# Optimization experiments

Measured on AMD Instinct MI355X. Metric: run time of the kernel, lower is better.

Reference implementation:

```python
import jax, jax.numpy as jnp
import numpy as np

N_NODE = 100000
HIDDEN = 128
BATCH = 4096
SESS_LEN = 50


def setup_inputs() -> dict:
    key = jax.random.key(0)
    k1, k2, k3, k4, k5 = jax.random.split(key, 5)
    return {
        "item_embedding": jax.random.normal(k1, (N_NODE, HIDDEN), dtype=jnp.float32),
        "items": jax.random.randint(k2, (BATCH, SESS_LEN), 0, N_NODE, dtype=jnp.int64),
        "A": jax.random.uniform(k3, (BATCH, BATCH), dtype=jnp.float32),
        "D": jax.random.uniform(k4, (BATCH, BATCH), dtype=jnp.float32),
        "target_embedding": jax.random.normal(k5, (BATCH, 1, 2 * HIDDEN), dtype=jnp.float32),
    }


def reference(item_embedding, items, A, D, target_embedding):
    # Gather per-session item embeddings: (batch, sess_len, hidden)
    seq_h = item_embedding[items]
    # Sum over session positions -> (batch, hidden)
    relation_emb = jnp.sum(seq_h, axis=1)
    # DA = D @ A, then propagate: (batch, batch) @ (batch, hidden)
    DA = jnp.matmul(D, A)
    relation_emb = jnp.matmul(DA, relation_emb)
    # Row-wise L2 normalization (torch.norm(dim=-1))
    norm = jnp.linalg.norm(relation_emb, axis=-1, keepdims=True)
    return relation_emb / norm
```

## Files before the change

### kernel.cpp

```cpp
#include <hip/hip_runtime.h>
#include <hip/hip_bf16.h>

#define BATCH   4096
#define HIDDEN  128
#define SESS    50
#define KTOT    4096
#define NB      ((size_t)BATCH * HIDDEN)

#define BK      128
#define NTILES  (KTOT / BK)
#define ABYTES  8192
#define BBYTES  32768
#define BUF     (ABYTES + BBYTES)

typedef __bf16 bf16x8 __attribute__((ext_vector_type(8)));
typedef __bf16 bf16x4 __attribute__((ext_vector_type(4)));
typedef float  f32x4  __attribute__((ext_vector_type(4)));

__device__ __forceinline__ f32x4 mfma_bf16(bf16x8 a, bf16x8 b, f32x4 c) {
    return __builtin_amdgcn_mfma_f32_16x16x32_bf16(a, b, c, 0, 0, 0);
}

__device__ __forceinline__ void gload16(const void* g, void* l) {
    __builtin_amdgcn_global_load_lds(
        (const __attribute__((address_space(1))) void*)g,
        (__attribute__((address_space(3))) void*)l, 16, 0, 0);
}


__global__ __launch_bounds__(256)
void gather_sum_kernel(const float* __restrict__ emb,
                       const int* __restrict__ items32,
                       __bf16* __restrict__ ETp) {
    __shared__ int sidx[4][SESS];
    const int t  = threadIdx.x;
    const int b0 = blockIdx.x * 4;
    const bool is64 = (items32[1] | items32[3] | items32[5] | items32[7] |
                       items32[9] | items32[11] | items32[13] | items32[15]) == 0;
    if (t < 4 * SESS) {
        const int w_ = t / SESS, s_ = t % SESS;
        sidx[w_][s_] = is64
            ? (int)((const long long*)items32)[(long)(b0 + w_) * SESS + s_]
            : items32[(b0 + w_) * SESS + s_];
    }
    __syncthreads();
    const int w    = t >> 6;
    const int lane = t & 63;
    const int c    = lane & 31;
    const int h    = lane >> 5;
    f32x4 acc = {0.f, 0.f, 0.f, 0.f};
#pragma unroll
    for (int i = 0; i < 25; ++i) {
        acc += *(const f32x4*)(emb + (long)sidx[w][h + 2 * i] * HIDDEN + c * 4);
    }
#pragma unroll
    for (int j = 0; j < 4; ++j) acc[j] += __shfl_xor(acc[j], 32, 64);
    if (h == 0) {
        const int  b     = b0 + w;
        const long chunk = b >> 3;
        const int  swz   = (int)((chunk & 3) << 4);
        char* basep = (char*)ETp + chunk * 2048 + (b & 7) * 2;
        const int hi4 = (c >> 2) * 256;
#pragma unroll
        for (int j = 0; j < 4; ++j) {
            const int hl = 4 * (c & 3) + j;
            *(__bf16*)(basep + ((hi4 + hl * 16) ^ swz)) = (__bf16)acc[j];
        }
    }
}

template <int PHASE>
__global__ __launch_bounds__(256, 1)
void gemm_mfma_kernel(const float* __restrict__ X,
                      const __bf16* __restrict__ Bpk,
                      __bf16* __restrict__ TTp,
                      float* __restrict__ out) {
    __shared__ __align__(16) char lds[3 * BUF];
    const int tid  = threadIdx.x;
    const int w    = tid >> 6;
    const int lane = tid & 63;
    const int lo   = lane & 15;
    const int quad = lane >> 4;
    const int rowBase = blockIdx.x * 16;

#define STAGE(t_, dst_) do {                                                 \
    _Pragma("unroll")                                                        \
    for (int oi_ = 0; oi_ < 2; ++oi_) {                                      \
        const int o_    = 2 * w + oi_;                                       \
        const int rloc_ = 2 * o_ + (lane >> 5);                              \
        gload16((const char*)X +                                             \
                    ((size_t)(rowBase + rloc_) * KTOT + (size_t)(t_) * BK) * 4 + \
                    (((lane & 31) * 16) ^ ((rloc_ & 7) << 4)),               \
                (dst_) + o_ * 1024);                                         \
    }                                                                        \
    _Pragma("unroll")                                                        \
    for (int bi_ = 0; bi_ < 8; ++bi_) {                                      \
        const int i_ = 8 * w + bi_;                                          \
        gload16((const char*)Bpk + (size_t)(t_) * BBYTES + i_ * 1024 +       \
                    lane * 16,                                               \
                (dst_) + ABYTES + i_ * 1024);                                \
    }                                                                        \
} while (0)

    f32x4 acc0 = {0.f, 0.f, 0.f, 0.f};
    f32x4 acc1 = {0.f, 0.f, 0.f, 0.f};

    const int akey = (lo & 7) << 4;
    const int bswz = quad << 4;
    const int bc0  = (int)(((2 * w) * 256 + lo * 16) ^ bswz);
    const int bc1  = (int)(((2 * w + 1) * 256 + lo * 16) ^ bswz);

#define KTILE(cb_) do {                                                      \
    const char* Ar_ = (cb_) + lo * 512;                                      \
    const char* Bb_ = (cb_) + ABYTES + quad * 2048;                          \
    _Pragma("unroll")                                                        \
    for (int ks_ = 0; ks_ < 4; ++ks_) {                                      \
        const f32x4 a0_ =                                                    \
            *(const f32x4*)(Ar_ + ((ks_ * 128 + quad * 32) ^ akey));         \
        const f32x4 a1_ =                                                    \
            *(const f32x4*)(Ar_ + ((ks_ * 128 + quad * 32 + 16) ^ akey));    \
        const bf16x8 b0_ = *(const bf16x8*)(Bb_ + ks_ * 8192 + bc0);         \
        const bf16x8 b1_ = *(const bf16x8*)(Bb_ + ks_ * 8192 + bc1);         \
        bf16x8 af_;                                                          \
        af_[0] = (__bf16)a0_[0]; af_[1] = (__bf16)a0_[1];                    \
        af_[2] = (__bf16)a0_[2]; af_[3] = (__bf16)a0_[3];                    \
        af_[4] = (__bf16)a1_[0]; af_[5] = (__bf16)a1_[1];                    \
        af_[6] = (__bf16)a1_[2]; af_[7] = (__bf16)a1_[3];                    \
        acc0 = mfma_bf16(af_, b0_, acc0);                                    \
        acc1 = mfma_bf16(af_, b1_, acc1);                                    \
    }                                                                        \
} while (0)

    STAGE(0, lds);
    STAGE(1, lds + BUF);

    char* cb = lds;
    char* sb = lds + 2 * BUF;
    for (int t = 0; t < NTILES; ++t) {
        if (t + 2 < NTILES) STAGE(t + 2, sb);
        if (t < NTILES - 2)
            asm volatile("s_waitcnt vmcnt(20)" ::: "memory");
        else if (t == NTILES - 2)
            asm volatile("s_waitcnt vmcnt(10)" ::: "memory");
        else
            asm volatile("s_waitcnt vmcnt(0)" ::: "memory");
        __builtin_amdgcn_s_barrier();
        __builtin_amdgcn_sched_barrier(0);
        KTILE(cb);
        __builtin_amdgcn_s_barrier();
        __builtin_amdgcn_sched_barrier(0);
        cb += BUF; if (cb == lds + 3 * BUF) cb = lds;
        sb += BUF; if (sb == lds + 3 * BUF) sb = lds;
    }
#undef KTILE
#undef STAGE

    if (PHASE == 1) {
        const long chunk = (rowBase >> 3) + (quad >> 1);
        const int  swz   = (int)((chunk & 3) << 4);
        char* tb = (char*)TTp + chunk * 2048 + (quad & 1) * 8;
        bf16x4 p0, p1;
#pragma unroll
        for (int r = 0; r < 4; ++r) {
            p0[r] = (__bf16)acc0[r];
            p1[r] = (__bf16)acc1[r];
        }
        *(bf16x4*)(tb + (((2 * w) * 256 + lo * 16) ^ swz))     = p0;
        *(bf16x4*)(tb + (((2 * w + 1) * 256 + lo * 16) ^ swz)) = p1;
    } else {
        __syncthreads();
        float (*Cs)[136] = (float (*)[136])lds;
#pragma unroll
        for (int r = 0; r < 4; ++r) {
            Cs[quad * 4 + r][(2 * w) * 16 + lo]     = acc0[r];
            Cs[quad * 4 + r][(2 * w + 1) * 16 + lo] = acc1[r];
        }
        __syncthreads();
        const int row = tid >> 4;
        const int cg  = tid & 15;
        const f32x4 c0 = *(const f32x4*)&Cs[row][cg * 8];
        const f32x4 c1 = *(const f32x4*)&Cs[row][cg * 8 + 4];
        float sq = c0[0] * c0[0] + c0[1] * c0[1] + c0[2] * c0[2] +
                   c0[3] * c0[3] + c1[0] * c1[0] + c1[1] * c1[1] +
                   c1[2] * c1[2] + c1[3] * c1[3];
#pragma unroll
        for (int m = 1; m < 16; m <<= 1) sq += __shfl_xor(sq, m, 64);
        const float s = rsqrtf(sq);
        float* op = out + (size_t)(rowBase + row) * HIDDEN + cg * 8;
        f32x4 o0, o1;
#pragma unroll
        for (int j = 0; j < 4; ++j) { o0[j] = c0[j] * s; o1[j] = c1[j] * s; }
        *(f32x4*)(op)     = o0;
        *(f32x4*)(op + 4) = o1;
    }
}

extern "C" void kernel_launch(void* const* d_in, const int* in_sizes, int n_in,
                              void* d_out, int out_size, void* d_ws, size_t ws_size,
                              hipStream_t stream) {
    const float* emb   = (const float*)d_in[0];
    const int*   items = (const int*)d_in[1];
    const float* A     = (const float*)d_in[2];
    const float* D     = (const float*)d_in[3];
    float* out = (float*)d_out;

    __bf16* ETp = (__bf16*)d_ws;
    __bf16* TTp = ETp + NB;

    gather_sum_kernel<<<BATCH / 4, 256, 0, stream>>>(emb, items, ETp);
    gemm_mfma_kernel<1><<<BATCH / 16, 256, 0, stream>>>(A, ETp, TTp, nullptr);
    gemm_mfma_kernel<2><<<BATCH / 16, 256, 0, stream>>>(D, TTp, nullptr, out);
}
```

Measured before the change: 207.9 us.

## Split-K GEMMs in two with 32-row tiles and separate reduce kernels

Each GEMM block now covers 32 output rows instead of 16, which halves how often the B operand is reloaded per row. Each wave computes a 16x64 subtile with four accumulators. The K dimension is split in two across blockIdx.y, which keeps the grid at 256 blocks and writes fp32 partial sums to workspace. Two new small kernels add the partials: one packs the intermediate to swizzled bf16 and the other applies the row L2 normalization. This costs two extra launches and an extra fp32 round-trip through global memory.

Measured after the change: 209.8 us. No clear change (+0.9%).

```diff
diff --git a/kernel.cpp b/kernel.cpp
--- a/kernel.cpp
+++ b/kernel.cpp
@@ -8,14 +8,15 @@
 #define NB      ((size_t)BATCH * HIDDEN)
 
 #define BK      128
-#define NTILES  (KTOT / BK)
-#define ABYTES  8192
+#define NT      16
+#define ABYTES  16384
 #define BBYTES  32768
 #define BUF     (ABYTES + BBYTES)
 
 typedef __bf16 bf16x8 __attribute__((ext_vector_type(8)));
 typedef __bf16 bf16x4 __attribute__((ext_vector_type(4)));
 typedef float  f32x4  __attribute__((ext_vector_type(4)));
+typedef float  f32x2  __attribute__((ext_vector_type(2)));
 
 __device__ __forceinline__ f32x4 mfma_bf16(bf16x8 a, bf16x8 b, f32x4 c) {
     return __builtin_amdgcn_mfma_f32_16x16x32_bf16(a, b, c, 0, 0, 0);
@@ -69,49 +70,50 @@
     }
 }
 
-template <int PHASE>
 __global__ __launch_bounds__(256, 1)
 void gemm_mfma_kernel(const float* __restrict__ X,
                       const __bf16* __restrict__ Bpk,
-                      __bf16* __restrict__ TTp,
-                      float* __restrict__ out) {
+                      float* __restrict__ Tpart) {
     __shared__ __align__(16) char lds[3 * BUF];
     const int tid  = threadIdx.x;
     const int w    = tid >> 6;
     const int lane = tid & 63;
     const int lo   = lane & 15;
     const int quad = lane >> 4;
-    const int rowBase = blockIdx.x * 16;
+    const int rowBase = blockIdx.x * 32;
+    const int kh      = blockIdx.y;
 
 #define STAGE(t_, dst_) do {                                                 \
     _Pragma("unroll")                                                        \
-    for (int oi_ = 0; oi_ < 2; ++oi_) {                                      \
-        const int o_    = 2 * w + oi_;                                       \
-        const int rloc_ = 2 * o_ + (lane >> 5);                              \
+    for (int ai_ = 0; ai_ < 4; ++ai_) {                                      \
+        const int i_    = 4 * w + ai_;                                       \
+        const int rloc_ = 2 * i_ + (lane >> 5);                              \
         gload16((const char*)X +                                             \
-                    ((size_t)(rowBase + rloc_) * KTOT + (size_t)(t_) * BK) * 4 + \
+                    ((size_t)(rowBase + rloc_) * KTOT + kh * 2048 +          \
+                     (size_t)(t_) * BK) * 4 +                                \
                     (((lane & 31) * 16) ^ ((rloc_ & 7) << 4)),               \
-                (dst_) + o_ * 1024);                                         \
+                (dst_) + i_ * 1024);                                         \
     }                                                                        \
     _Pragma("unroll")                                                        \
     for (int bi_ = 0; bi_ < 8; ++bi_) {                                      \
-        const int i_ = 8 * w + bi_;                                          \
-        gload16((const char*)Bpk + (size_t)(t_) * BBYTES + i_ * 1024 +       \
-                    lane * 16,                                               \
-                (dst_) + ABYTES + i_ * 1024);                                \
+        const int j_ = 8 * w + bi_;                                          \
+        gload16((const char*)Bpk + (size_t)kh * 524288 +                     \
+                    (size_t)(t_) * BBYTES + j_ * 1024 + lane * 16,           \
+                (dst_) + ABYTES + j_ * 1024);                                \
     }                                                                        \
 } while (0)
 
-    f32x4 acc0 = {0.f, 0.f, 0.f, 0.f};
-    f32x4 acc1 = {0.f, 0.f, 0.f, 0.f};
-
-    const int akey = (lo & 7) << 4;
-    const int bswz = quad << 4;
-    const int bc0  = (int)(((2 * w) * 256 + lo * 16) ^ bswz);
-    const int bc1  = (int)(((2 * w + 1) * 256 + lo * 16) ^ bswz);
+    f32x4 acc[4];
+#pragma unroll
+    for (int i = 0; i < 4; ++i) acc[i] = (f32x4){0.f, 0.f, 0.f, 0.f};
+
+    const int rbase = (w & 1) * 16;
+    const int ntb   = (w >> 1) * 4;
+    const int akey  = (lo & 7) << 4;
+    const int bkey  = quad << 4;
 
 #define KTILE(cb_) do {                                                      \
-    const char* Ar_ = (cb_) + lo * 512;                                      \
+    const char* Ar_ = (cb_) + (rbase + lo) * 512;                            \
     const char* Bb_ = (cb_) + ABYTES + quad * 2048;                          \
     _Pragma("unroll")                                                        \
     for (int ks_ = 0; ks_ < 4; ++ks_) {                                      \
@@ -119,15 +121,17 @@
             *(const f32x4*)(Ar_ + ((ks_ * 128 + quad * 32) ^ akey));         \
         const f32x4 a1_ =                                                    \
             *(const f32x4*)(Ar_ + ((ks_ * 128 + quad * 32 + 16) ^ akey));    \
-        const bf16x8 b0_ = *(const bf16x8*)(Bb_ + ks_ * 8192 + bc0);         \
-        const bf16x8 b1_ = *(const bf16x8*)(Bb_ + ks_ * 8192 + bc1);         \
         bf16x8 af_;                                                          \
         af_[0] = (__bf16)a0_[0]; af_[1] = (__bf16)a0_[1];                    \
         af_[2] = (__bf16)a0_[2]; af_[3] = (__bf16)a0_[3];                    \
         af_[4] = (__bf16)a1_[0]; af_[5] = (__bf16)a1_[1];                    \
         af_[6] = (__bf16)a1_[2]; af_[7] = (__bf16)a1_[3];                    \
-        acc0 = mfma_bf16(af_, b0_, acc0);                                    \
-        acc1 = mfma_bf16(af_, b1_, acc1);                                    \
+        _Pragma("unroll")                                                    \
+        for (int j_ = 0; j_ < 4; ++j_) {                                     \
+            const bf16x8 b_ = *(const bf16x8*)(Bb_ + ks_ * 8192 +            \
+                (((ntb + j_) * 256 + lo * 16) ^ bkey));                      \
+            acc[j_] = mfma_bf16(af_, b_, acc[j_]);                           \
+        }                                                                    \
     }                                                                        \
 } while (0)
 
@@ -136,12 +140,12 @@
 
     char* cb = lds;
     char* sb = lds + 2 * BUF;
-    for (int t = 0; t < NTILES; ++t) {
-        if (t + 2 < NTILES) STAGE(t + 2, sb);
-        if (t < NTILES - 2)
-            asm volatile("s_waitcnt vmcnt(20)" ::: "memory");
-        else if (t == NTILES - 2)
-            asm volatile("s_waitcnt vmcnt(10)" ::: "memory");
+    for (int t = 0; t < NT; ++t) {
+        if (t + 2 < NT) STAGE(t + 2, sb);
+        if (t < NT - 2)
+            asm volatile("s_waitcnt vmcnt(24)" ::: "memory");
+        else if (t == NT - 2)
+            asm volatile("s_waitcnt vmcnt(12)" ::: "memory");
         else
             asm volatile("s_waitcnt vmcnt(0)" ::: "memory");
         __builtin_amdgcn_s_barrier();
@@ -155,44 +159,49 @@
 #undef KTILE
 #undef STAGE
 
-    if (PHASE == 1) {
-        const long chunk = (rowBase >> 3) + (quad >> 1);
-        const int  swz   = (int)((chunk & 3) << 4);
-        char* tb = (char*)TTp + chunk * 2048 + (quad & 1) * 8;
-        bf16x4 p0, p1;
-#pragma unroll
-        for (int r = 0; r < 4; ++r) {
-            p0[r] = (__bf16)acc0[r];
-            p1[r] = (__bf16)acc1[r];
-        }
-        *(bf16x4*)(tb + (((2 * w) * 256 + lo * 16) ^ swz))     = p0;
-        *(bf16x4*)(tb + (((2 * w + 1) * 256 + lo * 16) ^ swz)) = p1;
-    } else {
-        __syncthreads();
-        float (*Cs)[136] = (float (*)[136])lds;
-#pragma unroll
-        for (int r = 0; r < 4; ++r) {
-            Cs[quad * 4 + r][(2 * w) * 16 + lo]     = acc0[r];
-            Cs[quad * 4 + r][(2 * w + 1) * 16 + lo] = acc1[r];
-        }
-        __syncthreads();
-        const int row = tid >> 4;
-        const int cg  = tid & 15;
-        const f32x4 c0 = *(const f32x4*)&Cs[row][cg * 8];
-        const f32x4 c1 = *(const f32x4*)&Cs[row][cg * 8 + 4];
-        float sq = c0[0] * c0[0] + c0[1] * c0[1] + c0[2] * c0[2] +
-                   c0[3] * c0[3] + c1[0] * c1[0] + c1[1] * c1[1] +
-                   c1[2] * c1[2] + c1[3] * c1[3];
-#pragma unroll
-        for (int m = 1; m < 16; m <<= 1) sq += __shfl_xor(sq, m, 64);
-        const float s = rsqrtf(sq);
-        float* op = out + (size_t)(rowBase + row) * HIDDEN + cg * 8;
-        f32x4 o0, o1;
-#pragma unroll
-        for (int j = 0; j < 4; ++j) { o0[j] = c0[j] * s; o1[j] = c1[j] * s; }
-        *(f32x4*)(op)     = o0;
-        *(f32x4*)(op + 4) = o1;
-    }
+    float* op = Tpart + (size_t)kh * NB +
+                (size_t)(rowBase + rbase) * HIDDEN;
+#pragma unroll
+    for (int r = 0; r < 4; ++r) {
+#pragma unroll
+        for (int j = 0; j < 4; ++j)
+            op[(quad * 4 + r) * HIDDEN + (ntb + j) * 16 + lo] = acc[j][r];
+    }
+}
+
+__global__ __launch_bounds__(256)
+void reduce2_kernel(const float* __restrict__ Tp, __bf16* __restrict__ TTp) {
+    const size_t i = ((size_t)blockIdx.x * 256 + threadIdx.x) * 4;
+    f32x4 a = *(const f32x4*)(Tp + i);
+    a += *(const f32x4*)(Tp + NB + i);
+    const int  b     = (int)(i >> 7);
+    const int  h0    = (int)(i & 127);
+    const long chunk = b >> 3;
+    const int  swz   = (int)((chunk & 3) << 4);
+    char* basep = (char*)TTp + chunk * 2048 + (b & 7) * 2;
+#pragma unroll
+    for (int j = 0; j < 4; ++j) {
+        const int h = h0 + j;
+        *(__bf16*)(basep + (((h >> 4) * 256 + (h & 15) * 16) ^ swz)) =
+            (__bf16)a[j];
+    }
+}
+
+__global__ __launch_bounds__(256)
+void reduce_norm_kernel(const float* __restrict__ Tp, float* __restrict__ out) {
+    const int t    = threadIdx.x;
+    const int w    = t >> 6;
+    const int lane = t & 63;
+    const int row  = blockIdx.x * 4 + w;
+    const size_t base = (size_t)row * HIDDEN + lane * 2;
+    f32x2 v = *(const f32x2*)(Tp + base);
+    v += *(const f32x2*)(Tp + NB + base);
+    float sq = v[0] * v[0] + v[1] * v[1];
+#pragma unroll
+    for (int m = 1; m < 64; m <<= 1) sq += __shfl_xor(sq, m, 64);
+    const float s = rsqrtf(sq);
+    f32x2 o = {v[0] * s, v[1] * s};
+    *(f32x2*)(out + base) = o;
 }
 
 extern "C" void kernel_launch(void* const* d_in, const int* in_sizes, int n_in,
@@ -206,8 +215,11 @@
 
     __bf16* ETp = (__bf16*)d_ws;
     __bf16* TTp = ETp + NB;
+    float*  Tp  = (float*)(TTp + NB);
 
     gather_sum_kernel<<<BATCH / 4, 256, 0, stream>>>(emb, items, ETp);
-    gemm_mfma_kernel<1><<<BATCH / 16, 256, 0, stream>>>(A, ETp, TTp, nullptr);
-    gemm_mfma_kernel<2><<<BATCH / 16, 256, 0, stream>>>(D, TTp, nullptr, out);
-}
+    gemm_mfma_kernel<<<dim3(BATCH / 32, 2), 256, 0, stream>>>(A, ETp, Tp);
+    reduce2_kernel<<<512, 256, 0, stream>>>(Tp, TTp);
+    gemm_mfma_kernel<<<dim3(BATCH / 32, 2), 256, 0, stream>>>(D, TTp, Tp);
+    reduce_norm_kernel<<<BATCH / 4, 256, 0, stream>>>(Tp, out);
+}
```

## Fuse gather and both GEMMs into one cooperative kernel with grid syncs

Applied to the files above, without the earlier changes.

Merges the gather-sum kernel and the two chained GEMMs into a single cooperative launch of 512 blocks, separated by grid-wide syncs. Each GEMM block now covers a 16x64 output tile instead of 16x128, which doubles the block count and allows two blocks per CU. The row normalization moves to a final phase that reads an fp32 intermediate buffer. This removes two kernel launch gaps and improves occupancy, at the cost of grid-sync overhead, an extra global round trip for the result, and re-reading the A/D rows twice (once per N-half).

Measured after the change: 592.8 us. +185.1%, slower.

```diff
diff --git a/kernel.cpp b/kernel.cpp
--- a/kernel.cpp
+++ b/kernel.cpp
@@ -1,5 +1,8 @@
 #include <hip/hip_runtime.h>
 #include <hip/hip_bf16.h>
+#include <hip/hip_cooperative_groups.h>
+
+namespace cg = cooperative_groups;
 
 #define BATCH   4096
 #define HIDDEN  128
@@ -8,14 +11,15 @@
 #define NB      ((size_t)BATCH * HIDDEN)
 
 #define BK      128
-#define NTILES  (KTOT / BK)
-#define ABYTES  8192
-#define BBYTES  32768
-#define BUF     (ABYTES + BBYTES)
+#define NT      (KTOT / BK)
+#define ABY     8192
+#define BBY     16384
+#define BUF     (ABY + BBY)
 
 typedef __bf16 bf16x8 __attribute__((ext_vector_type(8)));
 typedef __bf16 bf16x4 __attribute__((ext_vector_type(4)));
 typedef float  f32x4  __attribute__((ext_vector_type(4)));
+typedef float  f32x2  __attribute__((ext_vector_type(2)));
 
 __device__ __forceinline__ f32x4 mfma_bf16(bf16x8 a, bf16x8 b, f32x4 c) {
     return __builtin_amdgcn_mfma_f32_16x16x32_bf16(a, b, c, 0, 0, 0);
@@ -28,170 +32,174 @@
 }
 
 
-__global__ __launch_bounds__(256)
-void gather_sum_kernel(const float* __restrict__ emb,
-                       const int* __restrict__ items32,
-                       __bf16* __restrict__ ETp) {
-    __shared__ int sidx[4][SESS];
-    const int t  = threadIdx.x;
-    const int b0 = blockIdx.x * 4;
-    const bool is64 = (items32[1] | items32[3] | items32[5] | items32[7] |
-                       items32[9] | items32[11] | items32[13] | items32[15]) == 0;
-    if (t < 4 * SESS) {
-        const int w_ = t / SESS, s_ = t % SESS;
-        sidx[w_][s_] = is64
-            ? (int)((const long long*)items32)[(long)(b0 + w_) * SESS + s_]
-            : items32[(b0 + w_) * SESS + s_];
-    }
-    __syncthreads();
-    const int w    = t >> 6;
-    const int lane = t & 63;
-    const int c    = lane & 31;
-    const int h    = lane >> 5;
-    f32x4 acc = {0.f, 0.f, 0.f, 0.f};
-#pragma unroll
-    for (int i = 0; i < 25; ++i) {
-        acc += *(const f32x4*)(emb + (long)sidx[w][h + 2 * i] * HIDDEN + c * 4);
-    }
-#pragma unroll
-    for (int j = 0; j < 4; ++j) acc[j] += __shfl_xor(acc[j], 32, 64);
-    if (h == 0) {
-        const int  b     = b0 + w;
-        const long chunk = b >> 3;
-        const int  swz   = (int)((chunk & 3) << 4);
-        char* basep = (char*)ETp + chunk * 2048 + (b & 7) * 2;
-        const int hi4 = (c >> 2) * 256;
-#pragma unroll
-        for (int j = 0; j < 4; ++j) {
-            const int hl = 4 * (c & 3) + j;
-            *(__bf16*)(basep + ((hi4 + hl * 16) ^ swz)) = (__bf16)acc[j];
-        }
-    }
-}
-
 template <int PHASE>
-__global__ __launch_bounds__(256, 1)
-void gemm_mfma_kernel(const float* __restrict__ X,
-                      const __bf16* __restrict__ Bpk,
-                      __bf16* __restrict__ TTp,
-                      float* __restrict__ out) {
-    __shared__ __align__(16) char lds[3 * BUF];
-    const int tid  = threadIdx.x;
+__device__ __forceinline__ void gemm_block(const float* __restrict__ X,
+                                           const char* __restrict__ Bp,
+                                           char* lds, int tid, int blk,
+                                           __bf16* TTp, float* Rf) {
     const int w    = tid >> 6;
     const int lane = tid & 63;
     const int lo   = lane & 15;
     const int quad = lane >> 4;
-    const int rowBase = blockIdx.x * 16;
-
-#define STAGE(t_, dst_) do {                                                 \
+    const int mb   = blk >> 1;
+    const int nb   = blk & 1;
+    const int rowBase = mb * 16;
+    const int akey = (lo & 7) << 4;
+    f32x4 acc = {0.f, 0.f, 0.f, 0.f};
+
+#define STG(t_, dst_) do {                                                   \
     _Pragma("unroll")                                                        \
-    for (int oi_ = 0; oi_ < 2; ++oi_) {                                      \
-        const int o_    = 2 * w + oi_;                                       \
-        const int rloc_ = 2 * o_ + (lane >> 5);                              \
+    for (int ai_ = 0; ai_ < 2; ++ai_) {                                      \
+        const int rl_ = 4 * w + 2 * ai_ + (lane >> 5);                       \
         gload16((const char*)X +                                             \
-                    ((size_t)(rowBase + rloc_) * KTOT + (size_t)(t_) * BK) * 4 + \
-                    (((lane & 31) * 16) ^ ((rloc_ & 7) << 4)),               \
-                (dst_) + o_ * 1024);                                         \
+                    ((size_t)(rowBase + rl_) * KTOT + (size_t)(t_) * BK) * 4 \
+                    + (((lane & 31) * 16) ^ ((rl_ & 7) << 4)),               \
+                (dst_) + (4 * w + 2 * ai_) * 512);                           \
     }                                                                        \
     _Pragma("unroll")                                                        \
-    for (int bi_ = 0; bi_ < 8; ++bi_) {                                      \
-        const int i_ = 8 * w + bi_;                                          \
-        gload16((const char*)Bpk + (size_t)(t_) * BBYTES + i_ * 1024 +       \
+    for (int bi_ = 0; bi_ < 4; ++bi_) {                                      \
+        const int c_ = 4 * w + bi_;                                          \
+        gload16(Bp + ((size_t)(t_) * 16 + c_) * 2048 + nb * 1024 +           \
                     lane * 16,                                               \
-                (dst_) + ABYTES + i_ * 1024);                                \
+                (dst_) + ABY + c_ * 1024);                                   \
     }                                                                        \
 } while (0)
 
-    f32x4 acc0 = {0.f, 0.f, 0.f, 0.f};
-    f32x4 acc1 = {0.f, 0.f, 0.f, 0.f};
-
-    const int akey = (lo & 7) << 4;
-    const int bswz = quad << 4;
-    const int bc0  = (int)(((2 * w) * 256 + lo * 16) ^ bswz);
-    const int bc1  = (int)(((2 * w + 1) * 256 + lo * 16) ^ bswz);
-
-#define KTILE(cb_) do {                                                      \
+#define KTL(cb_) do {                                                        \
     const char* Ar_ = (cb_) + lo * 512;                                      \
-    const char* Bb_ = (cb_) + ABYTES + quad * 2048;                          \
+    const char* Bb_ = (cb_) + ABY + quad * 1024 + w * 256 +                  \
+                      ((lo * 16) ^ (quad << 4));                             \
     _Pragma("unroll")                                                        \
     for (int ks_ = 0; ks_ < 4; ++ks_) {                                      \
         const f32x4 a0_ =                                                    \
             *(const f32x4*)(Ar_ + ((ks_ * 128 + quad * 32) ^ akey));         \
         const f32x4 a1_ =                                                    \
             *(const f32x4*)(Ar_ + ((ks_ * 128 + quad * 32 + 16) ^ akey));    \
-        const bf16x8 b0_ = *(const bf16x8*)(Bb_ + ks_ * 8192 + bc0);         \
-        const bf16x8 b1_ = *(const bf16x8*)(Bb_ + ks_ * 8192 + bc1);         \
+        const bf16x8 b_ = *(const bf16x8*)(Bb_ + ks_ * 4096);                \
         bf16x8 af_;                                                          \
         af_[0] = (__bf16)a0_[0]; af_[1] = (__bf16)a0_[1];                    \
         af_[2] = (__bf16)a0_[2]; af_[3] = (__bf16)a0_[3];                    \
         af_[4] = (__bf16)a1_[0]; af_[5] = (__bf16)a1_[1];                    \
         af_[6] = (__bf16)a1_[2]; af_[7] = (__bf16)a1_[3];                    \
-        acc0 = mfma_bf16(af_, b0_, acc0);                                    \
-        acc1 = mfma_bf16(af_, b1_, acc1);                                    \
+        acc = mfma_bf16(af_, b_, acc);                                       \
     }                                                                        \
 } while (0)
 
-    STAGE(0, lds);
-    STAGE(1, lds + BUF);
-
+    STG(0, lds);
+    STG(1, lds + BUF);
     char* cb = lds;
     char* sb = lds + 2 * BUF;
-    for (int t = 0; t < NTILES; ++t) {
-        if (t + 2 < NTILES) STAGE(t + 2, sb);
-        if (t < NTILES - 2)
-            asm volatile("s_waitcnt vmcnt(20)" ::: "memory");
-        else if (t == NTILES - 2)
-            asm volatile("s_waitcnt vmcnt(10)" ::: "memory");
+    for (int t = 0; t < NT; ++t) {
+        if (t + 2 < NT) STG(t + 2, sb);
+        if (t < NT - 2)
+            asm volatile("s_waitcnt vmcnt(12)" ::: "memory");
+        else if (t == NT - 2)
+            asm volatile("s_waitcnt vmcnt(6)" ::: "memory");
         else
             asm volatile("s_waitcnt vmcnt(0)" ::: "memory");
         __builtin_amdgcn_s_barrier();
         __builtin_amdgcn_sched_barrier(0);
-        KTILE(cb);
+        KTL(cb);
         __builtin_amdgcn_s_barrier();
         __builtin_amdgcn_sched_barrier(0);
         cb += BUF; if (cb == lds + 3 * BUF) cb = lds;
         sb += BUF; if (sb == lds + 3 * BUF) sb = lds;
     }
-#undef KTILE
-#undef STAGE
-
-    if (PHASE == 1) {
+#undef STG
+#undef KTL
+
+    if constexpr (PHASE == 2) {
         const long chunk = (rowBase >> 3) + (quad >> 1);
         const int  swz   = (int)((chunk & 3) << 4);
         char* tb = (char*)TTp + chunk * 2048 + (quad & 1) * 8;
-        bf16x4 p0, p1;
-#pragma unroll
-        for (int r = 0; r < 4; ++r) {
-            p0[r] = (__bf16)acc0[r];
-            p1[r] = (__bf16)acc1[r];
+        bf16x4 p;
+#pragma unroll
+        for (int r = 0; r < 4; ++r) p[r] = (__bf16)acc[r];
+        *(bf16x4*)(tb + ((nb * 1024 + w * 256 + lo * 16) ^ swz)) = p;
+    } else {
+        float* op = Rf + (size_t)(rowBase + quad * 4) * HIDDEN +
+                    (nb * 4 + w) * 16 + lo;
+#pragma unroll
+        for (int r = 0; r < 4; ++r) op[(size_t)r * HIDDEN] = acc[r];
+    }
+}
+
+__global__ __launch_bounds__(256, 2)
+void mega_kernel(const float* __restrict__ emb,
+                 const int* __restrict__ items32,
+                 const float* __restrict__ Amat,
+                 const float* __restrict__ Dmat,
+                 __bf16* __restrict__ ETp,
+                 __bf16* __restrict__ TTp,
+                 float* __restrict__ Rf,
+                 float* __restrict__ out) {
+    __shared__ __align__(16) char lds[3 * BUF];
+    const int tid  = threadIdx.x;
+    const int blk  = blockIdx.x;
+    const int w    = tid >> 6;
+    const int lane = tid & 63;
+    cg::grid_group grid = cg::this_grid();
+
+    {
+        int* sidx = (int*)lds;
+        const int b0 = blk * 8;
+        const bool is64 = (items32[1] | items32[3] | items32[5] | items32[7] |
+                           items32[9] | items32[11] | items32[13] |
+                           items32[15]) == 0;
+        for (int i = tid; i < 8 * SESS; i += 256)
+            sidx[i] = is64
+                ? (int)((const long long*)items32)[(long)b0 * SESS + i]
+                : items32[b0 * SESS + i];
+        __syncthreads();
+        const int c  = lane & 31;
+        const int hh = lane >> 5;
+#pragma unroll
+        for (int rr = 0; rr < 2; ++rr) {
+            const int rloc = w * 2 + rr;
+            f32x4 acc = {0.f, 0.f, 0.f, 0.f};
+#pragma unroll
+            for (int i = 0; i < 25; ++i)
+                acc += *(const f32x4*)(emb +
+                        (long)sidx[rloc * SESS + hh + 2 * i] * HIDDEN + c * 4);
+#pragma unroll
+            for (int j = 0; j < 4; ++j) acc[j] += __shfl_xor(acc[j], 32, 64);
+            if (hh == 0) {
+                const int  b     = b0 + rloc;
+                const long chunk = b >> 3;
+                const int  swz   = (int)((chunk & 3) << 4);
+                char* basep = (char*)ETp + chunk * 2048 + (b & 7) * 2;
+                const int hi4 = (c >> 2) * 256;
+#pragma unroll
+                for (int j = 0; j < 4; ++j) {
+                    const int hl = 4 * (c & 3) + j;
+                    *(__bf16*)(basep + ((hi4 + hl * 16) ^ swz)) =
+                        (__bf16)acc[j];
+                }
+            }
         }
-        *(bf16x4*)(tb + (((2 * w) * 256 + lo * 16) ^ swz))     = p0;
-        *(bf16x4*)(tb + (((2 * w + 1) * 256 + lo * 16) ^ swz)) = p1;
-    } else {
-        __syncthreads();
-        float (*Cs)[136] = (float (*)[136])lds;
-#pragma unroll
-        for (int r = 0; r < 4; ++r) {
-            Cs[quad * 4 + r][(2 * w) * 16 + lo]     = acc0[r];
-            Cs[quad * 4 + r][(2 * w + 1) * 16 + lo] = acc1[r];
-        }
-        __syncthreads();
-        const int row = tid >> 4;
-        const int cg  = tid & 15;
-        const f32x4 c0 = *(const f32x4*)&Cs[row][cg * 8];
-        const f32x4 c1 = *(const f32x4*)&Cs[row][cg * 8 + 4];
-        float sq = c0[0] * c0[0] + c0[1] * c0[1] + c0[2] * c0[2] +
-                   c0[3] * c0[3] + c1[0] * c1[0] + c1[1] * c1[1] +
-                   c1[2] * c1[2] + c1[3] * c1[3];
-#pragma unroll
-        for (int m = 1; m < 16; m <<= 1) sq += __shfl_xor(sq, m, 64);
+        __threadfence();
+    }
+    grid.sync();
+
+    gemm_block<2>(Amat, (const char*)ETp, lds, tid, blk, TTp, nullptr);
+    __threadfence();
+    grid.sync();
+
+    gemm_block<3>(Dmat, (const char*)TTp, lds, tid, blk, nullptr, Rf);
+    __threadfence();
+    grid.sync();
+
+#pragma unroll
+    for (int rr = 0; rr < 2; ++rr) {
+        const int row = blk * 8 + w * 2 + rr;
+        const size_t base = (size_t)row * HIDDEN + lane * 2;
+        f32x2 v = *(const f32x2*)(Rf + base);
+        float sq = v[0] * v[0] + v[1] * v[1];
+#pragma unroll
+        for (int m = 1; m < 64; m <<= 1) sq += __shfl_xor(sq, m, 64);
         const float s = rsqrtf(sq);
-        float* op = out + (size_t)(rowBase + row) * HIDDEN + cg * 8;
-        f32x4 o0, o1;
-#pragma unroll
-        for (int j = 0; j < 4; ++j) { o0[j] = c0[j] * s; o1[j] = c1[j] * s; }
-        *(f32x4*)(op)     = o0;
-        *(f32x4*)(op + 4) = o1;
+        f32x2 o = {v[0] * s, v[1] * s};
+        *(f32x2*)(out + base) = o;
     }
 }
 
@@ -206,8 +214,10 @@
 
     __bf16* ETp = (__bf16*)d_ws;
     __bf16* TTp = ETp + NB;
-
-    gather_sum_kernel<<<BATCH / 4, 256, 0, stream>>>(emb, items, ETp);
-    gemm_mfma_kernel<1><<<BATCH / 16, 256, 0, stream>>>(A, ETp, TTp, nullptr);
-    gemm_mfma_kernel<2><<<BATCH / 16, 256, 0, stream>>>(D, TTp, nullptr, out);
-}
+    float*  Rf  = (float*)(TTp + NB);
+
+    void* args[] = { (void*)&emb, (void*)&items, (void*)&A, (void*)&D,
+                     (void*)&ETp, (void*)&TTp, (void*)&Rf, (void*)&out };
+    hipLaunchCooperativeKernel((void*)mega_kernel, dim3(512), dim3(256),
+                               args, 0, stream);
+}
```
